# Kernel optimization log

Measured on AMD Instinct MI355X. Metric: run time of the kernel, lower is better.

Reference implementation:

```python
import jax, jax.numpy as jnp
import numpy as np

B, T, D, K = 32, 2048, 1024, 31


def setup_inputs() -> dict:
    key = jax.random.key(0)
    ks = jax.random.split(key, 8)
    query = jax.random.normal(ks[0], (B, D), dtype=jnp.float32)
    memory = jax.random.normal(ks[1], (B, T, D), dtype=jnp.float32)
    prev_attn = jax.nn.softmax(jax.random.normal(ks[2], (B, T)), axis=-1).astype(jnp.float32)
    cum_attn = jax.random.uniform(ks[3], (B, T), dtype=jnp.float32)
    mask = jax.random.bernoulli(ks[4], 0.2, (B, T))
    mask = mask.at[:, 0].set(False)  # keep at least one valid position per row
    scale = 0.02
    Wq = jax.random.normal(ks[5], (D, D), dtype=jnp.float32) * scale    # torch Linear weight [out,in]
    Wm = jax.random.normal(ks[6], (D, D), dtype=jnp.float32) * scale
    k2 = jax.random.split(ks[7], 2)
    Wloc = jax.random.normal(k2[0], (D, 2, K), dtype=jnp.float32) * scale  # Conv1d weight [out_ch,in_ch,k]
    v = jax.random.normal(k2[1], (D,), dtype=jnp.float32) * scale          # Linear(d_model,1) weight squeezed
    return {"query": query, "memory": memory, "prev_attn": prev_attn,
            "cum_attn": cum_attn, "mask": mask,
            "Wq": Wq, "Wm": Wm, "Wloc": Wloc, "v": v}


def reference(query, memory, prev_attn, cum_attn, mask, Wq, Wm, Wloc, v):
    pad = Wloc.shape[-1] // 2
    # location features: [B,2,T] conv -> [B,D,T] -> [B,T,D]
    loc_in = jnp.stack([prev_attn, cum_attn], axis=1)
    loc = jax.lax.conv_general_dilated(
        loc_in, Wloc, window_strides=(1,), padding=[(pad, pad)],
        dimension_numbers=("NCW", "OIW", "NCW"))
    loc = jnp.transpose(loc, (0, 2, 1))                 # [B,T,D]
    q = (query @ Wq.T)[:, None, :]                      # [B,1,D]
    m = jnp.einsum("btd,ed->bte", memory, Wm)           # [B,T,D]
    e = jnp.einsum("btd,d->bt", jnp.tanh(q + m + loc), v)  # [B,T]
    e = jnp.where(mask, -jnp.inf, e)
    a = jax.nn.softmax(e, axis=1)                       # [B,T]
    ctx = jnp.einsum("bt,btd->bd", a, memory)           # [B,D]
    return ctx, a
```

## Files before the change

kernel.cpp:

```cpp
#include <hip/hip_runtime.h>
#include <math.h>

#define BATCH 32
#define T 2048
#define D 1024
#define KW 31
#define CPAD 15
#define KEXT 62
#define KEXTP 64
#define KTOT 1088
#define BM 128
#define BN 128
#define BK 32
#define NSTEP (KTOT / BK)

typedef __bf16 bf16_8 __attribute__((ext_vector_type(8)));
typedef __bf16 bf16_4 __attribute__((ext_vector_type(4)));
typedef float  f32x4  __attribute__((ext_vector_type(4)));

__device__ __forceinline__ float tanh_fast(float x) {
    return 1.f - 2.f * __builtin_amdgcn_rcpf(__expf(2.f * x) + 1.f);
}

__device__ __forceinline__ void glds16(const void* gsrc, void* ldst) {
    __builtin_amdgcn_global_load_lds(
        (const __attribute__((address_space(1))) unsigned int*)gsrc,
        (__attribute__((address_space(3))) unsigned int*)ldst, 16, 0, 0);
}

__global__ __launch_bounds__(256) void k_prep_b(const float* __restrict__ Wm,
                                                const float* __restrict__ Wloc,
                                                __bf16* __restrict__ Bext) {
    const int idx = blockIdx.x * 256 + threadIdx.x;
    const int d = idx / (KTOT / 4);
    const int kk = (idx % (KTOT / 4)) * 4;
    bf16_4 o;
    #pragma unroll
    for (int u = 0; u < 4; ++u) {
        const int k = kk + u;
        float val = 0.f;
        if (k < D) val = Wm[(size_t)d * D + k];
        else {
            const int j = k - D;
            if (j < KEXT) {
                const int c = (j >= KW) ? 1 : 0;
                const int kp = j - c * KW;
                val = Wloc[((size_t)d * 2 + c) * KW + kp];
            }
        }
        o[u] = (__bf16)val;
    }
    *(bf16_4*)(Bext + (size_t)d * KTOT + kk) = o;
}

__global__ __launch_bounds__(256) void k_prep_aloc(const float* __restrict__ prev,
                                                   const float* __restrict__ cum,
                                                   __bf16* __restrict__ Aloc) {
    const int idx = blockIdx.x * 256 + threadIdx.x;
    const int row = idx >> 4;
    const int j0 = (idx & 15) * 4;
    const int b = row >> 11;
    const int t = row & (T - 1);
    bf16_4 o;
    #pragma unroll
    for (int u = 0; u < 4; ++u) {
        const int j = j0 + u;
        float val = 0.f;
        if (j < KEXT) {
            const int c = (j >= KW) ? 1 : 0;
            const int kp = j - c * KW;
            const int ts = t + kp - CPAD;
            if (ts >= 0 && ts < T)
                val = (c ? cum : prev)[(size_t)b * T + ts];
        }
        o[u] = (__bf16)val;
    }
    *(bf16_4*)(Aloc + (size_t)row * KEXTP + j0) = o;
}

__global__ __launch_bounds__(256) void k_q(const float* __restrict__ query,
                                           const float* __restrict__ Wq,
                                           float* __restrict__ qout) {
    int b = blockIdx.y;
    int w = threadIdx.x >> 6;
    int lane = threadIdx.x & 63;
    int d = blockIdx.x * 4 + w;
    const float* qrow = query + (size_t)b * D;
    const float* wrow = Wq + (size_t)d * D;
    float s = 0.f;
    #pragma unroll
    for (int i = 0; i < D / 64; ++i) s += qrow[lane + i * 64] * wrow[lane + i * 64];
    #pragma unroll
    for (int off = 32; off > 0; off >>= 1) s += __shfl_down(s, off, 64);
    if (lane == 0) qout[(size_t)b * D + d] = s;
}

__global__ __launch_bounds__(256, 3) void k_gemm_e(
    const float* __restrict__ memory, const __bf16* __restrict__ Aloc,
    const __bf16* __restrict__ Bext, const float* __restrict__ qv,
    const float* __restrict__ vvec, float* __restrict__ e_part) {
    __shared__ bf16_8 As[3][512];
    __shared__ bf16_8 Bs[3][512];

    const int t0 = blockIdx.x * BM;
    const int d0 = blockIdx.y * BN;
    const int b  = blockIdx.z;
    const int tid  = threadIdx.x;
    const int lane = tid & 63;
    const int w    = tid >> 6;
    const int wr   = w >> 1, wc = w & 1;
    const int q    = lane >> 4, m = lane & 15;

    f32x4 acc[4][4] = {};

    const int g0 = w, g1 = w + 4;
    const size_t arow0 = (size_t)b * T + t0 + g0 * 16 + m;
    const size_t arow1 = (size_t)b * T + t0 + g1 * 16 + m;
    const float*  aptr0 = memory + arow0 * D + q * 8;
    const float*  aptr1 = memory + arow1 * D + q * 8;
    const __bf16* lptr0 = Aloc + arow0 * KEXTP + q * 8;
    const __bf16* lptr1 = Aloc + arow1 * KEXTP + q * 8;
    const __bf16* bptr0 = Bext + (size_t)(d0 + g0 * 16 + m) * KTOT + q * 8;
    const __bf16* bptr1 = Bext + (size_t)(d0 + g1 * 16 + m) * KTOT + q * 8;

    f32x4 pa[2][2];

    glds16(bptr0,      &Bs[0][g0 * 64]);
    glds16(bptr1,      &Bs[0][g1 * 64]);
    glds16(bptr0 + BK, &Bs[1][g0 * 64]);
    glds16(bptr1 + BK, &Bs[1][g1 * 64]);
    pa[0][0] = *(const f32x4*)(aptr0);
    pa[0][1] = *(const f32x4*)(aptr0 + 4);
    pa[1][0] = *(const f32x4*)(aptr1);
    pa[1][1] = *(const f32x4*)(aptr1 + 4);
    {
        bf16_8 c0, c1;
        #pragma unroll
        for (int i = 0; i < 4; ++i) {
            c0[i] = (__bf16)pa[0][0][i]; c0[i + 4] = (__bf16)pa[0][1][i];
            c1[i] = (__bf16)pa[1][0][i]; c1[i + 4] = (__bf16)pa[1][1][i];
        }
        As[0][g0 * 64 + lane] = c0;
        As[0][g1 * 64 + lane] = c1;
    }

    for (int k = 0; k < NSTEP; ++k) {
        const int p = k % 3;
        if (k > 0 && k * BK < D) {
            bf16_8 c0, c1;
            #pragma unroll
            for (int i = 0; i < 4; ++i) {
                c0[i] = (__bf16)pa[0][0][i]; c0[i + 4] = (__bf16)pa[0][1][i];
                c1[i] = (__bf16)pa[1][0][i]; c1[i + 4] = (__bf16)pa[1][1][i];
            }
            As[p][g0 * 64 + lane] = c0;
            As[p][g1 * 64 + lane] = c1;
        }
        __syncthreads();
        const int ka = k + 1;
        if (ka < NSTEP) {
            const int ka0 = ka * BK;
            if (ka0 < D) {
                pa[0][0] = *(const f32x4*)(aptr0 + ka0);
                pa[0][1] = *(const f32x4*)(aptr0 + ka0 + 4);
                pa[1][0] = *(const f32x4*)(aptr1 + ka0);
                pa[1][1] = *(const f32x4*)(aptr1 + ka0 + 4);
            } else {
                glds16(lptr0 + (ka0 - D), &As[ka % 3][g0 * 64]);
                glds16(lptr1 + (ka0 - D), &As[ka % 3][g1 * 64]);
            }
        }
        const int kb = k + 2;
        if (kb < NSTEP) {
            glds16(bptr0 + kb * BK, &Bs[kb % 3][g0 * 64]);
            glds16(bptr1 + kb * BK, &Bs[kb % 3][g1 * 64]);
        }
        bf16_8 af[4], bfr[4];
        #pragma unroll
        for (int i = 0; i < 4; ++i) af[i]  = As[p][(wr * 4 + i) * 64 + lane];
        #pragma unroll
        for (int j = 0; j < 4; ++j) bfr[j] = Bs[p][(wc * 4 + j) * 64 + lane];
        #pragma unroll
        for (int i = 0; i < 4; ++i)
            #pragma unroll
            for (int j = 0; j < 4; ++j)
                acc[i][j] = __builtin_amdgcn_mfma_f32_16x16x32_bf16(af[i], bfr[j], acc[i][j], 0, 0, 0);
    }

    float qreg[4], vreg[4];
    #pragma unroll
    for (int j = 0; j < 4; ++j) {
        const int d = d0 + wc * 64 + j * 16 + m;
        qreg[j] = qv[(size_t)b * D + d];
        vreg[j] = vvec[d];
    }
    const int dch = blockIdx.y * 2 + wc;
    #pragma unroll
    for (int i = 0; i < 4; ++i) {
        #pragma unroll
        for (int r = 0; r < 4; ++r) {
            float s = 0.f;
            #pragma unroll
            for (int j = 0; j < 4; ++j)
                s += tanh_fast(acc[i][j][r] + qreg[j]) * vreg[j];
            #pragma unroll
            for (int off = 8; off > 0; off >>= 1)
                s += __shfl_down(s, off, 16);
            if (m == 0) {
                const int t = t0 + wr * 64 + i * 16 + q * 4 + r;
                e_part[((size_t)b * T + t) * 16 + dch] = s;
            }
        }
    }
}

__global__ __launch_bounds__(256) void k_softmax(const float* __restrict__ e_part,
                                                 const int* __restrict__ mask,
                                                 float* __restrict__ aout) {
    const int b = blockIdx.x;
    const int tid = threadIdx.x;
    __shared__ float red[256];
    float ev[8];
    float lmax = -INFINITY;
    #pragma unroll
    for (int i = 0; i < 8; ++i) {
        const int t = tid + i * 256;
        const float* p = e_part + ((size_t)b * T + t) * 16;
        float s = 0.f;
        #pragma unroll
        for (int c = 0; c < 16; ++c) s += p[c];
        if (mask[(size_t)b * T + t] != 0) s = -INFINITY;
        ev[i] = s;
        lmax = fmaxf(lmax, s);
    }
    red[tid] = lmax; __syncthreads();
    for (int off = 128; off > 0; off >>= 1) {
        if (tid < off) red[tid] = fmaxf(red[tid], red[tid + off]);
        __syncthreads();
    }
    const float mx = red[0]; __syncthreads();
    float lsum = 0.f;
    #pragma unroll
    for (int i = 0; i < 8; ++i) {
        const float x = expf(ev[i] - mx);
        ev[i] = x;
        lsum += x;
    }
    red[tid] = lsum; __syncthreads();
    for (int off = 128; off > 0; off >>= 1) {
        if (tid < off) red[tid] += red[tid + off];
        __syncthreads();
    }
    const float inv = 1.f / red[0];
    #pragma unroll
    for (int i = 0; i < 8; ++i)
        aout[(size_t)b * T + tid + i * 256] = ev[i] * inv;
}

__global__ __launch_bounds__(256) void k_ctx_part(const float* __restrict__ memory,
                                                  const float* __restrict__ a,
                                                  float* __restrict__ ctx_part) {
    const int b = blockIdx.x;
    const int tc = blockIdx.y;
    const int d4 = threadIdx.x * 4;
    f32x4 acc = {0.f, 0.f, 0.f, 0.f};
    const float* mb = memory + ((size_t)b * T + (size_t)tc * 64) * D;
    const float* ab = a + (size_t)b * T + (size_t)tc * 64;
    #pragma unroll 4
    for (int t = 0; t < 64; ++t) {
        const float wgt = ab[t];
        const f32x4 m4 = *(const f32x4*)(mb + (size_t)t * D + d4);
        acc += wgt * m4;
    }
    *(f32x4*)(ctx_part + ((size_t)(b * 32 + tc)) * D + d4) = acc;
}

__global__ __launch_bounds__(256) void k_ctx_red(const float* __restrict__ ctx_part,
                                                 float* __restrict__ ctx) {
    const int idx = blockIdx.x * 256 + threadIdx.x;
    const int b = idx >> 10, d = idx & 1023;
    float s = 0.f;
    #pragma unroll
    for (int tc = 0; tc < 32; ++tc) s += ctx_part[((size_t)(b * 32 + tc)) * D + d];
    ctx[idx] = s;
}

extern "C" void kernel_launch(void* const* d_in, const int* in_sizes, int n_in,
                              void* d_out, int out_size, void* d_ws, size_t ws_size,
                              hipStream_t stream) {
    const float* query  = (const float*)d_in[0];
    const float* memory = (const float*)d_in[1];
    const float* prev   = (const float*)d_in[2];
    const float* cum    = (const float*)d_in[3];
    const int*   mask   = (const int*)d_in[4];
    const float* Wq     = (const float*)d_in[5];
    const float* Wm     = (const float*)d_in[6];
    const float* Wloc   = (const float*)d_in[7];
    const float* v      = (const float*)d_in[8];

    float* out = (float*)d_out;
    float* ctx = out;
    float* a   = out + BATCH * D;

    char* ws = (char*)d_ws;
    float*  qv       = (float*)(ws + 0);
    float*  e_part   = (float*)(ws + 131072);
    float*  ctx_part = (float*)(ws + 4325376);
    __bf16* Bext     = (__bf16*)(ws + 8519680);
    __bf16* Aloc     = (__bf16*)(ws + 10747904);

    k_prep_b<<<KTOT * D / (256 * 4), 256, 0, stream>>>(Wm, Wloc, Bext);
    k_prep_aloc<<<BATCH * T * 16 / 256, 256, 0, stream>>>(prev, cum, Aloc);
    k_q<<<dim3(D / 4, BATCH), 256, 0, stream>>>(query, Wq, qv);
    k_gemm_e<<<dim3(T / BM, D / BN, BATCH), 256, 0, stream>>>(memory, Aloc, Bext,
                                                              qv, v, e_part);
    k_softmax<<<BATCH, 256, 0, stream>>>(e_part, mask, a);
    k_ctx_part<<<dim3(BATCH, 32), 256, 0, stream>>>(memory, a, ctx_part);
    k_ctx_red<<<(BATCH * D) / 256, 256, 0, stream>>>(ctx_part, ctx);
}
```

Baseline: 757.0 us.

## Pre-convert memory to bf16 and use async LDS loads for both GEMM operands

Adds a prep kernel that converts the fp32 memory tensor to a bf16 buffer with the location-feature columns appended, so the GEMM reads one contiguous bf16 A operand. The GEMM loop then loads both A and B straight into LDS with global_load_lds, switching from a 3-stage buffer with register-staged fp32 conversion to a 2-stage double buffer, and raises the occupancy hint to 4. This takes conversion work and register pressure out of the main loop. The cost is an extra full pass over memory (read fp32, write bf16) and an extra sync per step.

```diff
diff --git a/kernel.cpp b/kernel.cpp
--- a/kernel.cpp
+++ b/kernel.cpp
@@ -7,7 +7,6 @@
 #define KW 31
 #define CPAD 15
 #define KEXT 62
-#define KEXTP 64
 #define KTOT 1088
 #define BM 128
 #define BN 128
@@ -53,9 +52,25 @@
     *(bf16_4*)(Bext + (size_t)d * KTOT + kk) = o;
 }
 
+__global__ __launch_bounds__(256) void k_prep_amem(const float* __restrict__ memory,
+                                                   __bf16* __restrict__ Amem) {
+    const int nvec = BATCH * T * (D / 8);
+    for (int idx = blockIdx.x * 256 + threadIdx.x; idx < nvec; idx += gridDim.x * 256) {
+        const int row = idx >> 7;
+        const int c = (idx & 127) * 8;
+        const float* src = memory + (size_t)row * D + c;
+        const f32x4 lo = *(const f32x4*)src;
+        const f32x4 hi = *(const f32x4*)(src + 4);
+        bf16_8 o;
+        #pragma unroll
+        for (int u = 0; u < 4; ++u) { o[u] = (__bf16)lo[u]; o[u + 4] = (__bf16)hi[u]; }
+        *(bf16_8*)(Amem + (size_t)row * KTOT + c) = o;
+    }
+}
+
 __global__ __launch_bounds__(256) void k_prep_aloc(const float* __restrict__ prev,
                                                    const float* __restrict__ cum,
-                                                   __bf16* __restrict__ Aloc) {
+                                                   __bf16* __restrict__ Amem) {
     const int idx = blockIdx.x * 256 + threadIdx.x;
     const int row = idx >> 4;
     const int j0 = (idx & 15) * 4;
@@ -75,7 +90,7 @@
         }
         o[u] = (__bf16)val;
     }
-    *(bf16_4*)(Aloc + (size_t)row * KEXTP + j0) = o;
+    *(bf16_4*)(Amem + (size_t)row * KTOT + D + j0) = o;
 }
 
 __global__ __launch_bounds__(256) void k_q(const float* __restrict__ query,
@@ -95,12 +110,12 @@
     if (lane == 0) qout[(size_t)b * D + d] = s;
 }
 
-__global__ __launch_bounds__(256, 3) void k_gemm_e(
-    const float* __restrict__ memory, const __bf16* __restrict__ Aloc,
-    const __bf16* __restrict__ Bext, const float* __restrict__ qv,
-    const float* __restrict__ vvec, float* __restrict__ e_part) {
-    __shared__ bf16_8 As[3][512];
-    __shared__ bf16_8 Bs[3][512];
+__global__ __launch_bounds__(256, 4) void k_gemm_e(
+    const __bf16* __restrict__ Amem, const __bf16* __restrict__ Bext,
+    const float* __restrict__ qv, const float* __restrict__ vvec,
+    float* __restrict__ e_part) {
+    __shared__ bf16_8 As[2][512];
+    __shared__ bf16_8 Bs[2][512];
 
     const int t0 = blockIdx.x * BM;
     const int d0 = blockIdx.y * BN;
@@ -114,77 +129,38 @@
     f32x4 acc[4][4] = {};
 
     const int g0 = w, g1 = w + 4;
-    const size_t arow0 = (size_t)b * T + t0 + g0 * 16 + m;
-    const size_t arow1 = (size_t)b * T + t0 + g1 * 16 + m;
-    const float*  aptr0 = memory + arow0 * D + q * 8;
-    const float*  aptr1 = memory + arow1 * D + q * 8;
-    const __bf16* lptr0 = Aloc + arow0 * KEXTP + q * 8;
-    const __bf16* lptr1 = Aloc + arow1 * KEXTP + q * 8;
+    const __bf16* aptr0 = Amem + ((size_t)b * T + t0 + g0 * 16 + m) * KTOT + q * 8;
+    const __bf16* aptr1 = Amem + ((size_t)b * T + t0 + g1 * 16 + m) * KTOT + q * 8;
     const __bf16* bptr0 = Bext + (size_t)(d0 + g0 * 16 + m) * KTOT + q * 8;
     const __bf16* bptr1 = Bext + (size_t)(d0 + g1 * 16 + m) * KTOT + q * 8;
 
-    f32x4 pa[2][2];
-
-    glds16(bptr0,      &Bs[0][g0 * 64]);
-    glds16(bptr1,      &Bs[0][g1 * 64]);
-    glds16(bptr0 + BK, &Bs[1][g0 * 64]);
-    glds16(bptr1 + BK, &Bs[1][g1 * 64]);
-    pa[0][0] = *(const f32x4*)(aptr0);
-    pa[0][1] = *(const f32x4*)(aptr0 + 4);
-    pa[1][0] = *(const f32x4*)(aptr1);
-    pa[1][1] = *(const f32x4*)(aptr1 + 4);
-    {
-        bf16_8 c0, c1;
+    glds16(aptr0, &As[0][g0 * 64]);
+    glds16(aptr1, &As[0][g1 * 64]);
+    glds16(bptr0, &Bs[0][g0 * 64]);
+    glds16(bptr1, &Bs[0][g1 * 64]);
+    __syncthreads();
+
+    for (int k = 0; k < NSTEP; ++k) {
+        const int p = k & 1;
+        const int kn = k + 1;
+        if (kn < NSTEP) {
+            const int kk = kn * BK;
+            glds16(aptr0 + kk, &As[p ^ 1][g0 * 64]);
+            glds16(aptr1 + kk, &As[p ^ 1][g1 * 64]);
+            glds16(bptr0 + kk, &Bs[p ^ 1][g0 * 64]);
+            glds16(bptr1 + kk, &Bs[p ^ 1][g1 * 64]);
+        }
+        bf16_8 bfr[4];
+        #pragma unroll
+        for (int j = 0; j < 4; ++j) bfr[j] = Bs[p][(wc * 4 + j) * 64 + lane];
         #pragma unroll
         for (int i = 0; i < 4; ++i) {
-            c0[i] = (__bf16)pa[0][0][i]; c0[i + 4] = (__bf16)pa[0][1][i];
-            c1[i] = (__bf16)pa[1][0][i]; c1[i + 4] = (__bf16)pa[1][1][i];
-        }
-        As[0][g0 * 64 + lane] = c0;
-        As[0][g1 * 64 + lane] = c1;
-    }
-
-    for (int k = 0; k < NSTEP; ++k) {
-        const int p = k % 3;
-        if (k > 0 && k * BK < D) {
-            bf16_8 c0, c1;
-            #pragma unroll
-            for (int i = 0; i < 4; ++i) {
-                c0[i] = (__bf16)pa[0][0][i]; c0[i + 4] = (__bf16)pa[0][1][i];
-                c1[i] = (__bf16)pa[1][0][i]; c1[i + 4] = (__bf16)pa[1][1][i];
-            }
-            As[p][g0 * 64 + lane] = c0;
-            As[p][g1 * 64 + lane] = c1;
-        }
-        __syncthreads();
-        const int ka = k + 1;
-        if (ka < NSTEP) {
-            const int ka0 = ka * BK;
-            if (ka0 < D) {
-                pa[0][0] = *(const f32x4*)(aptr0 + ka0);
-                pa[0][1] = *(const f32x4*)(aptr0 + ka0 + 4);
-                pa[1][0] = *(const f32x4*)(aptr1 + ka0);
-                pa[1][1] = *(const f32x4*)(aptr1 + ka0 + 4);
-            } else {
-                glds16(lptr0 + (ka0 - D), &As[ka % 3][g0 * 64]);
-                glds16(lptr1 + (ka0 - D), &As[ka % 3][g1 * 64]);
-            }
-        }
-        const int kb = k + 2;
-        if (kb < NSTEP) {
-            glds16(bptr0 + kb * BK, &Bs[kb % 3][g0 * 64]);
-            glds16(bptr1 + kb * BK, &Bs[kb % 3][g1 * 64]);
-        }
-        bf16_8 af[4], bfr[4];
-        #pragma unroll
-        for (int i = 0; i < 4; ++i) af[i]  = As[p][(wr * 4 + i) * 64 + lane];
-        #pragma unroll
-        for (int j = 0; j < 4; ++j) bfr[j] = Bs[p][(wc * 4 + j) * 64 + lane];
-        #pragma unroll
-        for (int i = 0; i < 4; ++i)
+            const bf16_8 af = As[p][(wr * 4 + i) * 64 + lane];
             #pragma unroll
             for (int j = 0; j < 4; ++j)
-                acc[i][j] = __builtin_amdgcn_mfma_f32_16x16x32_bf16(af[i], bfr[j], acc[i][j], 0, 0, 0);
+                acc[i][j] = __builtin_amdgcn_mfma_f32_16x16x32_bf16(af, bfr[j], acc[i][j], 0, 0, 0);
+        }
+        __syncthreads();
     }
 
     float qreg[4], vreg[4];
@@ -307,13 +283,13 @@
     float*  e_part   = (float*)(ws + 131072);
     float*  ctx_part = (float*)(ws + 4325376);
     __bf16* Bext     = (__bf16*)(ws + 8519680);
-    __bf16* Aloc     = (__bf16*)(ws + 10747904);
+    __bf16* Amem     = (__bf16*)(ws + 10747904);
 
     k_prep_b<<<KTOT * D / (256 * 4), 256, 0, stream>>>(Wm, Wloc, Bext);
-    k_prep_aloc<<<BATCH * T * 16 / 256, 256, 0, stream>>>(prev, cum, Aloc);
+    k_prep_amem<<<8192, 256, 0, stream>>>(memory, Amem);
+    k_prep_aloc<<<BATCH * T * 16 / 256, 256, 0, stream>>>(prev, cum, Amem);
     k_q<<<dim3(D / 4, BATCH), 256, 0, stream>>>(query, Wq, qv);
-    k_gemm_e<<<dim3(T / BM, D / BN, BATCH), 256, 0, stream>>>(memory, Aloc, Bext,
-                                                              qv, v, e_part);
+    k_gemm_e<<<dim3(T / BM, D / BN, BATCH), 256, 0, stream>>>(Amem, Bext, qv, v, e_part);
     k_softmax<<<BATCH, 256, 0, stream>>>(e_part, mask, a);
     k_ctx_part<<<dim3(BATCH, 32), 256, 0, stream>>>(memory, a, ctx_part);
     k_ctx_red<<<(BATCH * D) / 256, 256, 0, stream>>>(ctx_part, ctx);
```

After: 732.4 us. 1.03x faster.
